# Kernel tuning notes

Measured on AMD Instinct MI355X. Metric: run time of the kernel, lower is better.

## Reference

```python
import jax, jax.numpy as jnp
import numpy as np

B, V, T = 256, 4, 512
N = 128          # num_notes_per_voice[0]
H = 256          # lstm_hidden_size
HL = 200         # hidden_size_linear
L = 2            # num_layers


def _scalar_lstm_last(x, Wih, Whh, b):
    """Stacked LSTM(input=1, hidden=1, layers=L) over x:(M,T) -> last output (M,).
    Wih, Whh, b: (L, 4) scalar weights per gate (i,f,g,o order, PyTorch biases summed)."""
    M = x.shape[0]
    h0 = jnp.zeros((L, M), x.dtype)
    c0 = jnp.zeros((L, M), x.dtype)

    def step(carry, xt):
        h, c = carry
        inp = xt
        hs, cs = [], []
        for l in range(L):
            g = Wih[l][:, None] * inp[None, :] + Whh[l][:, None] * h[l][None, :] + b[l][:, None]  # (4, M)
            i, f, gg, o = jax.nn.sigmoid(g[0]), jax.nn.sigmoid(g[1]), jnp.tanh(g[2]), jax.nn.sigmoid(g[3])
            cn = f * c[l] + i * gg
            hn = o * jnp.tanh(cn)
            hs.append(hn); cs.append(cn)
            inp = hn
        return (jnp.stack(hs), jnp.stack(cs)), None

    (h, _), _ = jax.lax.scan(step, (h0, c0), x.T)  # scan over time
    return h[-1]  # top layer final hidden, (M,)


def _lstm2_last(x, Wih0, Whh0, b0, Wih1, Whh1, b1):
    """2-layer LSTM(input=1, hidden=H) over x:(B,S,1) -> last top-layer hidden (B,H)."""
    Bs = x.shape[0]
    Hd = Whh0.shape[1]

    def cell(pre, c):
        i, f, g, o = jnp.split(pre, 4, axis=-1)
        cn = jax.nn.sigmoid(f) * c + jax.nn.sigmoid(i) * jnp.tanh(g)
        return jax.nn.sigmoid(o) * jnp.tanh(cn), cn

    z = jnp.zeros((Bs, Hd), x.dtype)

    def step(carry, xt):
        h0, c0, h1, c1 = carry
        h0n, c0n = cell(xt @ Wih0.T + h0 @ Whh0.T + b0, c0)
        h1n, c1n = cell(h0n @ Wih1.T + h1 @ Whh1.T + b1, c1)
        return (h0n, c0n, h1n, c1n), None

    (_, _, h1, _), _ = jax.lax.scan(step, (z, z, z, z), x.transpose(1, 0, 2))
    return h1


def _branch(tokens, tW, tU, tb, Wih0, Whh0, b0, Wih1, Whh1, b1):
    """Fused version of the per-class Python loop: one-hot each of N classes over
    time (voice 0 only, as in the source), run scalar LSTM per (batch, class),
    then 2-layer LSTM over the class axis. tokens: (B, T) int."""
    Bs, Ts = tokens.shape
    onehot = (tokens[:, :, None] == jnp.arange(N)[None, None, :]).astype(jnp.float32)  # (B,T,N)
    x = onehot.transpose(0, 2, 1).reshape(Bs * N, Ts)           # (B*N, T): one series per class
    states = _scalar_lstm_last(x, tW, tU, tb).reshape(Bs, N, 1)  # States_ln / States_rn
    return _lstm2_last(states, Wih0, Whh0, b0, Wih1, Whh1, b1)   # (B, H)


def setup_inputs() -> dict:
    key = jax.random.key(0)
    ks = iter(jax.random.split(key, 32))
    def rn_(shape, s=0.1):
        return jax.random.normal(next(ks), shape, dtype=jnp.float32) * s
    inp = {
        "ln": jax.random.randint(next(ks), (B, V, T), 0, N),
        "cn": jax.random.randint(next(ks), (B, V - 1), 0, N),
        "rn": jax.random.randint(next(ks), (B, V, T), 0, N),
        "metas": jax.random.randint(next(ks), (B, 3, T), 0, 16),
        # time_lstm_left/right: LSTM(1->1), L layers; biases summed into one
        "tl_Wih": rn_((L, 4), 0.5), "tl_Whh": rn_((L, 4), 0.5), "tl_b": rn_((L, 4), 0.5),
        "tr_Wih": rn_((L, 4), 0.5), "tr_Whh": rn_((L, 4), 0.5), "tr_b": rn_((L, 4), 0.5),
        # notes_lstm_left/right: 2-layer LSTM(1->H)
        "nl_Wih0": rn_((4 * H, 1)), "nl_Whh0": rn_((4 * H, H)), "nl_b0": rn_((4 * H,)),
        "nl_Wih1": rn_((4 * H, H)), "nl_Whh1": rn_((4 * H, H)), "nl_b1": rn_((4 * H,)),
        "nr_Wih0": rn_((4 * H, 1)), "nr_Whh0": rn_((4 * H, H)), "nr_b0": rn_((4 * H,)),
        "nr_Wih1": rn_((4 * H, H)), "nr_Whh1": rn_((4 * H, H)), "nr_b1": rn_((4 * H,)),
        # mlp_predictions: Linear(2H -> HL) -> ReLU -> Linear(HL -> N)
        "mW1": rn_((HL, 2 * H)), "mb1": rn_((HL,)),
        "mW2": rn_((N, HL)), "mb2": rn_((N,)),
    }
    return inp


def reference(ln, cn, rn, metas,
              tl_Wih, tl_Whh, tl_b, tr_Wih, tr_Whh, tr_b,
              nl_Wih0, nl_Whh0, nl_b0, nl_Wih1, nl_Whh1, nl_b1,
              nr_Wih0, nr_Whh0, nr_b0, nr_Wih1, nr_Whh1, nr_b1,
              mW1, mb1, mW2, mb2):
    # cn and metas are unpacked but unused in the original forward()
    note_pred_ln = _branch(ln[:, 0, :], tl_Wih, tl_Whh, tl_b,
                           nl_Wih0, nl_Whh0, nl_b0, nl_Wih1, nl_Whh1, nl_b1)
    note_pred_rn = _branch(rn[:, 0, :], tr_Wih, tr_Whh, tr_b,
                           nr_Wih0, nr_Whh0, nr_b0, nr_Wih1, nr_Whh1, nr_b1)
    h = jnp.concatenate([note_pred_ln, note_pred_rn], axis=1)   # (B, 2H)
    return jax.nn.relu(h @ mW1.T + mb1) @ mW2.T + mb2           # (B, N)
```

## Files before the change

kernel.cpp:

```cpp
#include <hip/hip_runtime.h>


typedef _Float16 f16;
typedef __attribute__((ext_vector_type(4))) _Float16 f16x4;
typedef __attribute__((ext_vector_type(8))) _Float16 f16x8;
typedef __attribute__((ext_vector_type(4))) float f32x4;
typedef unsigned long long u64;

#define NBATCH 256
#define NTIME  512
#define NCLS   128
#define NHID   256

__device__ __forceinline__ float sigf(float x) {
    return __builtin_amdgcn_rcpf(1.0f + __expf(-x));
}
__device__ __forceinline__ float tanh_f(float x) {
    return fmaf(2.0f, __builtin_amdgcn_rcpf(1.0f + __expf(-2.0f * x)), -1.0f);
}
__device__ __forceinline__ f16x4 LO(f16x8 v) { f16x4 r; r[0]=v[0]; r[1]=v[1]; r[2]=v[2]; r[3]=v[3]; return r; }
__device__ __forceinline__ f16x4 HI(f16x8 v) { f16x4 r; r[0]=v[4]; r[1]=v[5]; r[2]=v[6]; r[3]=v[7]; return r; }

__device__ __forceinline__ u64 ld_llc(const u64* p) {
    return __hip_atomic_load(p, __ATOMIC_RELAXED, __HIP_MEMORY_SCOPE_AGENT);
}
__device__ __forceinline__ void st_llc(u64* p, u64 v) {
    __hip_atomic_store(p, v, __ATOMIC_RELAXED, __HIP_MEMORY_SCOPE_AGENT);
}
__device__ __forceinline__ int ld_flag(const int* p) {
    return __hip_atomic_load(p, __ATOMIC_RELAXED, __HIP_MEMORY_SCOPE_AGENT);
}
__device__ __forceinline__ void st_flag(int* p, int v) {
    __hip_atomic_store(p, v, __ATOMIC_RELAXED, __HIP_MEMORY_SCOPE_AGENT);
}

struct P6 {
    const float* s0; const float* s1; const float* s2;
    const float* s3; const float* s4; const float* s5;
};

__global__ __launch_bounds__(256) void k_pre(
    const int* __restrict__ ln, const int* __restrict__ rn,
    const float* __restrict__ tlW, const float* __restrict__ tlU, const float* __restrict__ tlb,
    const float* __restrict__ trW, const float* __restrict__ trU, const float* __restrict__ trb,
    float* __restrict__ states,
    P6 p, f16* __restrict__ wdst,
    int* __restrict__ flags)
{
    const int bid = blockIdx.x;
    const int tid = threadIdx.x;
    if (bid >= 768) {
        int* f = flags + (bid - 768) * 16384;
        for (int i = tid; i < 16384; i += 256) f[i] = 0;
        return;
    }
    if (bid >= 256) {
        const int base = (bid - 256) * 3072;
#pragma unroll
        for (int k = 0; k < 12; ++k) {
            const int i = base + k * 256 + tid;
            const int seg = i >> 18, d = i & 262143;
            const float* s = seg == 0 ? p.s0 : seg == 1 ? p.s1 : seg == 2 ? p.s2
                           : seg == 3 ? p.s3 : seg == 4 ? p.s4 : p.s5;
            const int e  = d & 7;
            const int fr = (d >> 3) & 15;
            const int fq = (d >> 7) & 3;
            const int ktp = (d >> 9) & 7;
            const int fi = (d >> 12) & 15;
            const int g  = (d >> 16) & 3;
            const int row = g * 256 + fi * 16 + fr;
            const int col = ktp * 32 + (e >> 2) * 16 + fq * 4 + (e & 3);
            wdst[i] = (f16)s[row * 256 + col];
        }
        return;
    }
    __shared__ int tok[2][NTIME];
    const int half = tid >> 7, n = tid & 127;
    const int pair = bid * 2 + half;
    const int branch = pair >> 8;
    const int b = pair & 255;
    const int* tp = (branch ? rn : ln) + (size_t)b * (4 * NTIME);
    for (int i = n; i < NTIME; i += 128) tok[half][i] = tp[i];
    __syncthreads();
    const float* W  = branch ? trW : tlW;
    const float* U  = branch ? trU : tlU;
    const float* Bb = branch ? trb : tlb;
    const float u00 = U[0], u01 = U[1], u02 = U[2], u03 = U[3];
    const float f00 = Bb[0], f01 = Bb[1], f02 = Bb[2], f03 = Bb[3];
    const float o00 = f00 + W[0], o01 = f01 + W[1], o02 = f02 + W[2], o03 = f03 + W[3];
    const float w10 = W[4], w11 = W[5], w12 = W[6], w13 = W[7];
    const float u10 = U[4], u11 = U[5], u12 = U[6], u13 = U[7];
    const float b10 = Bb[4], b11 = Bb[5], b12 = Bb[6], b13 = Bb[7];
    float h0 = 0.f, c0 = 0.f, h1 = 0.f, c1 = 0.f;
    {
        const bool x = (tok[half][0] == n);
        float pi = fmaf(u00, h0, x ? o00 : f00);
        float pf = fmaf(u01, h0, x ? o01 : f01);
        float pg = fmaf(u02, h0, x ? o02 : f02);
        float po = fmaf(u03, h0, x ? o03 : f03);
        const float ig = sigf(pi), fg = sigf(pf), gg = tanh_f(pg), og = sigf(po);
        c0 = fmaf(fg, c0, ig * gg);
        h0 = og * tanh_f(c0);
    }
    for (int t = 1; t < NTIME; ++t) {
        const bool x = (tok[half][t] == n);
        float api = fmaf(u00, h0, x ? o00 : f00);
        float apf = fmaf(u01, h0, x ? o01 : f01);
        float apg = fmaf(u02, h0, x ? o02 : f02);
        float apo = fmaf(u03, h0, x ? o03 : f03);
        float bpi = fmaf(w10, h0, fmaf(u10, h1, b10));
        float bpf = fmaf(w11, h0, fmaf(u11, h1, b11));
        float bpg = fmaf(w12, h0, fmaf(u12, h1, b12));
        float bpo = fmaf(w13, h0, fmaf(u13, h1, b13));
        const float aig = sigf(api), afg = sigf(apf), agg = tanh_f(apg), aog = sigf(apo);
        const float big = sigf(bpi), bfg = sigf(bpf), bgg = tanh_f(bpg), bog = sigf(bpo);
        c0 = fmaf(afg, c0, aig * agg);
        c1 = fmaf(bfg, c1, big * bgg);
        h0 = aog * tanh_f(c0);
        h1 = bog * tanh_f(c1);
    }
    {
        float pi = fmaf(w10, h0, fmaf(u10, h1, b10));
        float pf = fmaf(w11, h0, fmaf(u11, h1, b11));
        float pg = fmaf(w12, h0, fmaf(u12, h1, b12));
        float po = fmaf(w13, h0, fmaf(u13, h1, b13));
        const float ig = sigf(pi), fg = sigf(pf), gg = tanh_f(pg), og = sigf(po);
        c1 = fmaf(fg, c1, ig * gg);
        h1 = og * tanh_f(c1);
    }
    states[((size_t)(branch * NBATCH + b)) * NCLS + n] = h1;
}

__global__ __launch_bounds__(256, 2) void k_rec(
    const float* __restrict__ states,
    const f16* __restrict__ whh0, const f16* __restrict__ whh1,
    const f16* __restrict__ wih1,
    const float* __restrict__ wih0L, const float* __restrict__ wih0R,
    const float* __restrict__ b0L, const float* __restrict__ b0R,
    const float* __restrict__ b1L, const float* __restrict__ b1R,
    f16* __restrict__ h0img,
    f16* __restrict__ ring,
    int* __restrict__ flags0,
    int* __restrict__ flags1,
    float* __restrict__ h1out)
{
    extern __shared__ char smem[];
    f16*   wlds = (f16*)smem;
    f16*   img  = (f16*)(smem + 65536);
    float* cmb  = (float*)(smem + 73728);

    const int bid = blockIdx.x;
    const bool isL1 = bid >= 256;
    const int sub = isL1 ? (bid - 256) : bid;
    const int qm = sub >> 5, g = sub & 31;
    const int branch = g >> 4, tb = g & 15;
    const int tid = threadIdx.x;
    const int w = tid >> 6, l = tid & 63, fr = l & 15, fq = l >> 4;

    {
        const f16* base = (isL1 ? whh1 : whh0) + ((size_t)branch << 18);
        for (int c = tid; c < 4096; c += 256) {
            const int rl = c >> 6, coli = c & 63;
            const int gg = rl >> 4, ff = (rl >> 3) & 1, ktp = rl & 7;
            *(uint4*)(wlds + rl * 512 + coli * 8) =
                *(const uint4*)(base + ((size_t)((gg * 16 + qm * 2 + ff) * 8 + ktp) << 9) + coli * 8);
        }
    }
    ((uint4*)img)[tid] = (uint4){0u, 0u, 0u, 0u};
    ((uint4*)img)[tid + 256] = (uint4){0u, 0u, 0u, 0u};

    if (!isL1) {
        const float* bias = branch ? b0R : b0L;
        const float* w0p  = branch ? wih0R : wih0L;
        const int fi_f = qm * 2 + (w < 2 ? w : 0);
        float bv[4], w0v[4];
#pragma unroll
        for (int g4 = 0; g4 < 4; ++g4) {
            bv[g4]  = bias[g4 * 256 + fi_f * 16 + fr];
            w0v[g4] = w0p[g4 * 256 + fi_f * 16 + fr];
        }
        float cst[4] = {0.f, 0.f, 0.f, 0.f};
        f16* gimg = h0img + (size_t)g * (NCLS * 4096);
        int* f0 = flags0 + g * 512;
        __syncthreads();

        for (int s = 0; s < NCLS; ++s) {
            float st[4];
            if (w < 2) {
#pragma unroll
                for (int r = 0; r < 4; ++r)
                    st[r] = states[((size_t)(branch * NBATCH + tb * 16 + fq * 4 + r)) * NCLS + s];
            }
            f16x4 af[16];
#pragma unroll
            for (int kt = 0; kt < 16; ++kt)
                af[kt] = *(const f16x4*)(img + kt * 256 + l * 4);
            f32x4 acc[2];
#pragma unroll
            for (int f = 0; f < 2; ++f) {
                f32x4 a0 = {0.f,0.f,0.f,0.f}, a1 = {0.f,0.f,0.f,0.f};
#pragma unroll
                for (int ktp = 0; ktp < 8; ++ktp) {
                    const f16x8 v = *(const f16x8*)(wlds + (((w * 2 + f) * 8 + ktp) << 9) + l * 8);
                    a0 = __builtin_amdgcn_mfma_f32_16x16x16f16(af[2 * ktp],     LO(v), a0, 0, 0, 0);
                    a1 = __builtin_amdgcn_mfma_f32_16x16x16f16(af[2 * ktp + 1], HI(v), a1, 0, 0, 0);
                }
                acc[f] = a0 + a1;
            }
            if (w == 0) {
#pragma unroll
                for (int r = 0; r < 4; ++r) cmb[(0 * 4 + r) * 64 + l] = acc[1][r];
            } else if (w == 1) {
#pragma unroll
                for (int r = 0; r < 4; ++r) cmb[(1 * 4 + r) * 64 + l] = acc[0][r];
            } else if (w == 2) {
#pragma unroll
                for (int r = 0; r < 4; ++r) {
                    cmb[(2 * 4 + r) * 64 + l] = acc[0][r];
                    cmb[(3 * 4 + r) * 64 + l] = acc[1][r];
                }
            } else {
#pragma unroll
                for (int r = 0; r < 4; ++r) {
                    cmb[(4 * 4 + r) * 64 + l] = acc[0][r];
                    cmb[(5 * 4 + r) * 64 + l] = acc[1][r];
                }
            }
            __syncthreads();
            if (w < 2) {
#pragma unroll
                for (int r = 0; r < 4; ++r) {
                    const float g0 = (w == 0) ? acc[0][r] : cmb[(0 * 4 + r) * 64 + l];
                    const float g1 = (w == 0) ? cmb[(1 * 4 + r) * 64 + l] : acc[1][r];
                    const float g2 = (w == 0) ? cmb[(2 * 4 + r) * 64 + l] : cmb[(3 * 4 + r) * 64 + l];
                    const float g3 = (w == 0) ? cmb[(4 * 4 + r) * 64 + l] : cmb[(5 * 4 + r) * 64 + l];
                    const float pi = fmaf(st[r], w0v[0], g0 + bv[0]);
                    const float pf = fmaf(st[r], w0v[1], g1 + bv[1]);
                    const float pg = fmaf(st[r], w0v[2], g2 + bv[2]);
                    const float po = fmaf(st[r], w0v[3], g3 + bv[3]);
                    const float ig = sigf(pi), fg = sigf(pf), gg = tanh_f(pg), og = sigf(po);
                    cst[r] = fmaf(fg, cst[r], ig * gg);
                    const float hn = og * tanh_f(cst[r]);
                    img[fi_f * 256 + (fq * 4 + r + 16 * (fr >> 2)) * 4 + (fr & 3)] = (f16)hn;
                }
            }
            __syncthreads();
            if (w == 0) {
                u64* gd = (u64*)(gimg + (size_t)s * 4096);
                st_llc(gd + qm * 128 + l,      ((const u64*)img)[qm * 128 + l]);
                st_llc(gd + qm * 128 + 64 + l, ((const u64*)img)[qm * 128 + 64 + l]);
                asm volatile("s_waitcnt vmcnt(0)" ::: "memory");
                if (l == 0) st_flag(f0 + qm * 64, s + 1);
            } else if (w == 2 && s < NCLS - 1 && l < 7) {
                const int p = l + (l >= qm);
                while (ld_flag(f0 + p * 64) <= s) __builtin_amdgcn_s_sleep(1);
            }
            if (s == NCLS - 1) break;
            __syncthreads();
            if (tid < 128) {
                const u64* gs = (const u64*)(gimg + (size_t)s * 4096);
                u64 tmp[7];
#pragma unroll
                for (int j = 0; j < 7; ++j) {
                    const int p = j + (j >= qm);
                    tmp[j] = ld_llc(gs + p * 128 + tid);
                }
#pragma unroll
                for (int j = 0; j < 7; ++j) {
                    const int p = j + (j >= qm);
                    ((u64*)img)[p * 128 + tid] = tmp[j];
                }
            }
            __syncthreads();
        }
    } else {
        const float* bias = branch ? b1R : b1L;
        const int fi_f = qm * 2 + (w < 2 ? w : 0);
        float bv[4];
#pragma unroll
        for (int g4 = 0; g4 < 4; ++g4) bv[g4] = bias[g4 * 256 + fi_f * 16 + fr];
        float cst[4] = {0.f, 0.f, 0.f, 0.f};
        const f16* wstream = wih1 + ((size_t)branch << 18) + l * 8;
        const f16* gimg = h0img + (size_t)g * (NCLS * 4096);
        f16* gring = ring + (size_t)g * (4 * 4096);
        int* f0 = flags0 + g * 512;
        int* f1 = flags1 + g * 512;
        __syncthreads();
        if (w == 3 && l < 8) {
            while (ld_flag(f0 + l * 64) < 1) __builtin_amdgcn_s_sleep(2);
        }
        __syncthreads();
        f16x4 af0[16];
        {
            const u64* s2 = (const u64*)gimg + l;
#pragma unroll
            for (int kt = 0; kt < 16; ++kt)
                af0[kt] = __builtin_bit_cast(f16x4, ld_llc(s2 + kt * 64));
        }

        for (int t = 0; t < NCLS; ++t) {
            f16x8 wv[2][8];
#pragma unroll
            for (int f = 0; f < 2; ++f)
#pragma unroll
                for (int ktp = 0; ktp < 8; ++ktp)
                    wv[f][ktp] = *(const f16x8*)(wstream
                        + ((size_t)((w * 16 + qm * 2 + f) * 8 + ktp) << 9));
            f16x4 af1[16];
#pragma unroll
            for (int kt = 0; kt < 16; ++kt)
                af1[kt] = *(const f16x4*)(img + kt * 256 + l * 4);
            f32x4 acc[2];
#pragma unroll
            for (int f = 0; f < 2; ++f) {
                f32x4 a0 = {0.f,0.f,0.f,0.f}, a1 = {0.f,0.f,0.f,0.f};
#pragma unroll
                for (int ktp = 0; ktp < 8; ++ktp) {
                    const f16x8 v = *(const f16x8*)(wlds + (((w * 2 + f) * 8 + ktp) << 9) + l * 8);
                    a0 = __builtin_amdgcn_mfma_f32_16x16x16f16(af1[2 * ktp],     LO(v), a0, 0, 0, 0);
                    a1 = __builtin_amdgcn_mfma_f32_16x16x16f16(af1[2 * ktp + 1], HI(v), a1, 0, 0, 0);
                }
#pragma unroll
                for (int ktp = 0; ktp < 8; ++ktp) {
                    a0 = __builtin_amdgcn_mfma_f32_16x16x16f16(af0[2 * ktp],     LO(wv[f][ktp]), a0, 0, 0, 0);
                    a1 = __builtin_amdgcn_mfma_f32_16x16x16f16(af0[2 * ktp + 1], HI(wv[f][ktp]), a1, 0, 0, 0);
                }
                acc[f] = a0 + a1;
            }
            if (w == 0) {
#pragma unroll
                for (int r = 0; r < 4; ++r) cmb[(3 * 4 + r) * 64 + l] = acc[1][r];
            } else if (w == 1) {
#pragma unroll
                for (int r = 0; r < 4; ++r) cmb[(0 * 4 + r) * 64 + l] = acc[0][r];
            } else if (w == 2) {
#pragma unroll
                for (int r = 0; r < 4; ++r) {
                    cmb[(1 * 4 + r) * 64 + l] = acc[0][r];
                    cmb[(4 * 4 + r) * 64 + l] = acc[1][r];
                }
            } else {
#pragma unroll
                for (int r = 0; r < 4; ++r) {
                    cmb[(2 * 4 + r) * 64 + l] = acc[0][r];
                    cmb[(5 * 4 + r) * 64 + l] = acc[1][r];
                }
            }
            __syncthreads();
            if (w < 2) {
#pragma unroll
                for (int r = 0; r < 4; ++r) {
                    const float g0 = (w == 0) ? acc[0][r] : cmb[(3 * 4 + r) * 64 + l];
                    const float g1 = (w == 0) ? cmb[(0 * 4 + r) * 64 + l] : acc[1][r];
                    const float g2 = (w == 0) ? cmb[(1 * 4 + r) * 64 + l] : cmb[(4 * 4 + r) * 64 + l];
                    const float g3 = (w == 0) ? cmb[(2 * 4 + r) * 64 + l] : cmb[(5 * 4 + r) * 64 + l];
                    const float pi = g0 + bv[0];
                    const float pf = g1 + bv[1];
                    const float pg = g2 + bv[2];
                    const float po = g3 + bv[3];
                    const float ig = sigf(pi), fg = sigf(pf), gg = tanh_f(pg), og = sigf(po);
                    cst[r] = fmaf(fg, cst[r], ig * gg);
                    const float hn = og * tanh_f(cst[r]);
                    if (t == NCLS - 1)
                        h1out[((size_t)(branch * NBATCH + tb * 16 + fq * 4 + r)) * NHID
                              + fi_f * 16 + fr] = hn;
                    else
                        img[fi_f * 256 + (fq * 4 + r + 16 * (fr >> 2)) * 4 + (fr & 3)] = (f16)hn;
                }
            }
            if (t == NCLS - 1) break;
            __syncthreads();
            f16* slot = gring + (size_t)(t & 3) * 4096;
            if (w == 0) {
                u64* gd = (u64*)slot;
                st_llc(gd + qm * 128 + l,      ((const u64*)img)[qm * 128 + l]);
                st_llc(gd + qm * 128 + 64 + l, ((const u64*)img)[qm * 128 + 64 + l]);
                asm volatile("s_waitcnt vmcnt(0)" ::: "memory");
                if (l == 0) st_flag(f1 + qm * 64, t + 1);
            } else if (w == 2 && l < 7) {
                const int p = l + (l >= qm);
                while (ld_flag(f1 + p * 64) <= t) __builtin_amdgcn_s_sleep(1);
            } else if (w == 3 && l < 8) {
                while (ld_flag(f0 + l * 64) < t + 2) __builtin_amdgcn_s_sleep(1);
            }
            __syncthreads();
            {
                const u64* s2 = (const u64*)(gimg + (size_t)(t + 1) * 4096) + l;
#pragma unroll
                for (int kt = 0; kt < 16; ++kt)
                    af0[kt] = __builtin_bit_cast(f16x4, ld_llc(s2 + kt * 64));
            }
            if (tid < 128) {
                const u64* gs = (const u64*)slot;
                u64 tmp[7];
#pragma unroll
                for (int j = 0; j < 7; ++j) {
                    const int p = j + (j >= qm);
                    tmp[j] = ld_llc(gs + p * 128 + tid);
                }
#pragma unroll
                for (int j = 0; j < 7; ++j) {
                    const int p = j + (j >= qm);
                    ((u64*)img)[p * 128 + tid] = tmp[j];
                }
            }
            __syncthreads();
        }
    }
}

__global__ __launch_bounds__(256) void k_mlp(
    const float* __restrict__ h1all,
    const float* __restrict__ W1, const float* __restrict__ b1,
    const float* __restrict__ W2, const float* __restrict__ b2,
    float* __restrict__ out)
{
    __shared__ float hrow[512];
    __shared__ float hid[200];
    const int b = blockIdx.x, tid = threadIdx.x;
    hrow[tid]       = h1all[(size_t)b * NHID + tid];
    hrow[256 + tid] = h1all[(size_t)(NBATCH + b) * NHID + tid];
    __syncthreads();
    if (tid < 200) {
        float a = b1[tid];
        const float* wr = W1 + (size_t)tid * 512;
        for (int k = 0; k < 512; ++k) a = fmaf(wr[k], hrow[k], a);
        hid[tid] = fmaxf(a, 0.f);
    }
    __syncthreads();
    if (tid < 128) {
        float a = b2[tid];
        const float* wr = W2 + (size_t)tid * 200;
        for (int j = 0; j < 200; ++j) a = fmaf(wr[j], hid[j], a);
        out[(size_t)b * 128 + tid] = a;
    }
}

extern "C" void kernel_launch(void* const* d_in, const int* in_sizes, int n_in,
                              void* d_out, int out_size, void* d_ws, size_t ws_size,
                              hipStream_t stream)
{
    (void)in_sizes; (void)n_in; (void)out_size; (void)ws_size;
    const int*   ln    = (const int*)d_in[0];
    const int*   rn    = (const int*)d_in[2];
    const float* tlW   = (const float*)d_in[4];
    const float* tlU   = (const float*)d_in[5];
    const float* tlb   = (const float*)d_in[6];
    const float* trW   = (const float*)d_in[7];
    const float* trU   = (const float*)d_in[8];
    const float* trb   = (const float*)d_in[9];
    const float* wih0L = (const float*)d_in[10];
    const float* b0L   = (const float*)d_in[12];
    const float* b1L   = (const float*)d_in[15];
    const float* wih0R = (const float*)d_in[16];
    const float* b0R   = (const float*)d_in[18];
    const float* b1R   = (const float*)d_in[21];
    const float* mW1   = (const float*)d_in[22];
    const float* mb1   = (const float*)d_in[23];
    const float* mW2   = (const float*)d_in[24];
    const float* mb2   = (const float*)d_in[25];

    char* ws = (char*)d_ws;
    f16*   w16    = (f16*)ws;
    float* states = (float*)(ws + 3145728);
    float* h1out  = (float*)(ws + 3407872);
    int*   flags  = (int*)(ws + 3932160);
    f16*   ring   = (f16*)(ws + 4063232);
    f16*   h0img  = (f16*)(ws + 5111808);

    f16* whh0 = w16;
    f16* whh1 = w16 + 2 * 262144;
    f16* wih1 = w16 + 4 * 262144;
    int* flags0 = flags;
    int* flags1 = flags + 16384;

    (void)hipFuncSetAttribute(reinterpret_cast<const void*>(k_rec),
                              hipFuncAttributeMaxDynamicSharedMemorySize, 79872);

    P6 p { (const float*)d_in[11], (const float*)d_in[17],
           (const float*)d_in[14], (const float*)d_in[20],
           (const float*)d_in[13], (const float*)d_in[19] };
    k_pre<<<770, 256, 0, stream>>>(ln, rn, tlW, tlU, tlb, trW, trU, trb,
                                   states, p, w16, flags);
    k_rec<<<512, 256, 79872, stream>>>(states, whh0, whh1, wih1, wih0L, wih0R,
                                       b0L, b0R, b1L, b1R, h0img, ring,
                                       flags0, flags1, h1out);
    k_mlp<<<256, 256, 0, stream>>>(h1out, mW1, mb1, mW2, mb2, (float*)d_out);
}
```

Before: 602.0 us.

## Load recurrent hidden state straight from global, drop LDS staging and barrier

Each step now reads its A-operand fragments (the previous hidden state of layer 0 and layer 1) directly from the agent-scope global images, instead of first copying the peer slices into the LDS img buffer behind an extra __syncthreads. This removes one block barrier and an LDS round-trip from every step of the serial recurrence. Flag polling also switches from sleep-based spinning to a tight double-load spin, which lowers wake-up latency at the cost of more memory traffic. A risk is that each lane now issues more global loads on the critical path, and that the unchanged local hidden slice written into img must still match what is read back from global.

Measured after the change: 589.9 us. -2.0%, faster.

```diff
diff --git a/kernel.cpp b/kernel.cpp
--- a/kernel.cpp
+++ b/kernel.cpp
@@ -32,6 +32,11 @@
 }
 __device__ __forceinline__ void st_flag(int* p, int v) {
     __hip_atomic_store(p, v, __ATOMIC_RELAXED, __HIP_MEMORY_SCOPE_AGENT);
+}
+__device__ __forceinline__ void poll_ge(const int* p, int target) {
+    int a = ld_flag(p);
+    int b = ld_flag(p);
+    while (a < target) { a = b; b = ld_flag(p); }
 }
 
 struct P6 {
@@ -185,16 +190,23 @@
         __syncthreads();
 
         for (int s = 0; s < NCLS; ++s) {
+            f16x4 af[16];
+            if (s == 0) {
+#pragma unroll
+                for (int kt = 0; kt < 16; ++kt)
+                    af[kt] = __builtin_bit_cast(f16x4, 0ull);
+            } else {
+                const u64* gs = (const u64*)(gimg + (size_t)(s - 1) * 4096) + l;
+#pragma unroll
+                for (int kt = 0; kt < 16; ++kt)
+                    af[kt] = __builtin_bit_cast(f16x4, ld_llc(gs + kt * 64));
+            }
             float st[4];
             if (w < 2) {
 #pragma unroll
                 for (int r = 0; r < 4; ++r)
                     st[r] = states[((size_t)(branch * NBATCH + tb * 16 + fq * 4 + r)) * NCLS + s];
             }
-            f16x4 af[16];
-#pragma unroll
-            for (int kt = 0; kt < 16; ++kt)
-                af[kt] = *(const f16x4*)(img + kt * 256 + l * 4);
             f32x4 acc[2];
 #pragma unroll
             for (int f = 0; f < 2; ++f) {
@@ -253,24 +265,9 @@
                 if (l == 0) st_flag(f0 + qm * 64, s + 1);
             } else if (w == 2 && s < NCLS - 1 && l < 7) {
                 const int p = l + (l >= qm);
-                while (ld_flag(f0 + p * 64) <= s) __builtin_amdgcn_s_sleep(1);
+                poll_ge(f0 + p * 64, s + 1);
             }
             if (s == NCLS - 1) break;
-            __syncthreads();
-            if (tid < 128) {
-                const u64* gs = (const u64*)(gimg + (size_t)s * 4096);
-                u64 tmp[7];
-#pragma unroll
-                for (int j = 0; j < 7; ++j) {
-                    const int p = j + (j >= qm);
-                    tmp[j] = ld_llc(gs + p * 128 + tid);
-                }
-#pragma unroll
-                for (int j = 0; j < 7; ++j) {
-                    const int p = j + (j >= qm);
-                    ((u64*)img)[p * 128 + tid] = tmp[j];
-                }
-            }
             __syncthreads();
         }
     } else {
@@ -287,18 +284,29 @@
         int* f1 = flags1 + g * 512;
         __syncthreads();
         if (w == 3 && l < 8) {
-            while (ld_flag(f0 + l * 64) < 1) __builtin_amdgcn_s_sleep(2);
+            poll_ge(f0 + l * 64, 1);
         }
         __syncthreads();
-        f16x4 af0[16];
-        {
-            const u64* s2 = (const u64*)gimg + l;
-#pragma unroll
-            for (int kt = 0; kt < 16; ++kt)
-                af0[kt] = __builtin_bit_cast(f16x4, ld_llc(s2 + kt * 64));
-        }
 
         for (int t = 0; t < NCLS; ++t) {
+            f16x4 af0[16];
+            {
+                const u64* s2 = (const u64*)(gimg + (size_t)t * 4096) + l;
+#pragma unroll
+                for (int kt = 0; kt < 16; ++kt)
+                    af0[kt] = __builtin_bit_cast(f16x4, ld_llc(s2 + kt * 64));
+            }
+            f16x4 af1[16];
+            if (t == 0) {
+#pragma unroll
+                for (int kt = 0; kt < 16; ++kt)
+                    af1[kt] = __builtin_bit_cast(f16x4, 0ull);
+            } else {
+                const u64* gs = (const u64*)(gring + (size_t)((t - 1) & 3) * 4096) + l;
+#pragma unroll
+                for (int kt = 0; kt < 16; ++kt)
+                    af1[kt] = __builtin_bit_cast(f16x4, ld_llc(gs + kt * 64));
+            }
             f16x8 wv[2][8];
 #pragma unroll
             for (int f = 0; f < 2; ++f)
@@ -306,10 +314,6 @@
                 for (int ktp = 0; ktp < 8; ++ktp)
                     wv[f][ktp] = *(const f16x8*)(wstream
                         + ((size_t)((w * 16 + qm * 2 + f) * 8 + ktp) << 9));
-            f16x4 af1[16];
-#pragma unroll
-            for (int kt = 0; kt < 16; ++kt)
-                af1[kt] = *(const f16x4*)(img + kt * 256 + l * 4);
             f32x4 acc[2];
 #pragma unroll
             for (int f = 0; f < 2; ++f) {
@@ -379,30 +383,9 @@
                 if (l == 0) st_flag(f1 + qm * 64, t + 1);
             } else if (w == 2 && l < 7) {
                 const int p = l + (l >= qm);
-                while (ld_flag(f1 + p * 64) <= t) __builtin_amdgcn_s_sleep(1);
+                poll_ge(f1 + p * 64, t + 1);
             } else if (w == 3 && l < 8) {
-                while (ld_flag(f0 + l * 64) < t + 2) __builtin_amdgcn_s_sleep(1);
-            }
-            __syncthreads();
-            {
-                const u64* s2 = (const u64*)(gimg + (size_t)(t + 1) * 4096) + l;
-#pragma unroll
-                for (int kt = 0; kt < 16; ++kt)
-                    af0[kt] = __builtin_bit_cast(f16x4, ld_llc(s2 + kt * 64));
-            }
-            if (tid < 128) {
-                const u64* gs = (const u64*)slot;
-                u64 tmp[7];
-#pragma unroll
-                for (int j = 0; j < 7; ++j) {
-                    const int p = j + (j >= qm);
-                    tmp[j] = ld_llc(gs + p * 128 + tid);
-                }
-#pragma unroll
-                for (int j = 0; j < 7; ++j) {
-                    const int p = j + (j >= qm);
-                    ((u64*)img)[p * 128 + tid] = tmp[j];
-                }
+                poll_ge(f0 + l * 64, t + 2);
             }
             __syncthreads();
         }
```
